# Performance work log

Hardware: AMD Instinct MI355X
Metric: run time of the kernel (lower is better)

Reference implementation:

```python
import jax, jax.numpy as jnp
import numpy as np


def _ragged_reverse(x, lengths):
    # x: [N, L, C]; flip the first `lengths[n]` steps of each sample, zero-fill the rest.
    N, L, C = x.shape
    t = jnp.arange(L, dtype=lengths.dtype)[None, :]          # [1, L]
    Ln = lengths[:, None]                                     # [N, 1]
    valid = t < Ln                                            # [N, L]
    idx = jnp.where(valid, Ln - 1 - t, 0)                     # [N, L]
    rev = jnp.take_along_axis(x, idx[:, :, None], axis=1)     # [N, L, C]
    return jnp.where(valid[:, :, None], rev, jnp.zeros((), x.dtype))


def _gru(xb, W_ih, W_hh, b_ih, b_hh):
    # xb: [B, L, C] -> outputs [B, L, H] (standard torch GRU cell math).
    B, L, C = xb.shape
    H = W_hh.shape[0]
    xw = xb @ W_ih + b_ih                                     # [B, L, 3H], input proj done once

    def step(h, xw_t):
        gh = h @ W_hh + b_hh                                  # [B, 3H]
        xr, xz, xn = jnp.split(xw_t, 3, axis=-1)
        hr, hz, hn = jnp.split(gh, 3, axis=-1)
        r = jax.nn.sigmoid(xr + hr)
        z = jax.nn.sigmoid(xz + hz)
        n = jnp.tanh(xn + r * hn)
        h_new = (1.0 - z) * n + z * h
        return h_new, h_new

    h0 = jnp.zeros((B, H), xb.dtype)
    _, ys = jax.lax.scan(step, h0, jnp.swapaxes(xw, 0, 1))    # ys: [L, B, H]
    return jnp.swapaxes(ys, 0, 1)                             # [B, L, H]


def reference(x, lengths, W_ih, W_hh, b_ih, b_hh):
    N, L, C = x.shape
    # to_bidirection: stack [forward; ragged-reversed] along batch -> [2N, L, C]
    rev = _ragged_reverse(x, lengths)
    xb = jnp.concatenate([x, rev], axis=0)
    out = _gru(xb, W_ih, W_hh, b_ih, b_hh)                    # [2N, L, H]
    # from_bidirection: split halves, concat on feature dim -> [N, L, 2H]
    return jnp.concatenate([out[:N], out[N:]], axis=2)


def setup_inputs() -> dict:
    key = jax.random.key(0)
    ks = jax.random.split(key, 6)
    N, L, C, H = 32, 2048, 64, 128
    s = 1.0 / np.sqrt(H)
    return {
        "x": jax.random.normal(ks[0], (N, L, C), dtype=jnp.float32),
        "lengths": jax.random.randint(ks[1], (N,), 1, L + 1, dtype=jnp.int32),
        "W_ih": jax.random.normal(ks[2], (C, 3 * H), dtype=jnp.float32) * s,
        "W_hh": jax.random.normal(ks[3], (H, 3 * H), dtype=jnp.float32) * s,
        "b_ih": jax.random.normal(ks[4], (3 * H,), dtype=jnp.float32) * s,
        "b_hh": jax.random.normal(ks[5], (3 * H,), dtype=jnp.float32) * s,
    }
```

## Files before the change

kernel.cpp:

```cpp
#include <hip/hip_runtime.h>

#define L_SEQ 2048
#define C_IN  64
#define HH    128
#define NSEQ  32
#define B2    64
#define G3    384
#define T_TILE 128

typedef _Float16 half2_t __attribute__((ext_vector_type(2)));

#define PINU(v) asm volatile("" : "+v"(v))

__device__ __forceinline__ float fdot2u(unsigned int a, unsigned int b, float c) {
    return __builtin_amdgcn_fdot2(__builtin_bit_cast(half2_t, a),
                                  __builtin_bit_cast(half2_t, b), c, false);
}

__device__ __forceinline__ unsigned int pack_h2(float a, float b) {
    half2_t t; t.x = (_Float16)a; t.y = (_Float16)b;
    return __builtin_bit_cast(unsigned int, t);
}

__device__ __forceinline__ float qadd1(float x) {
    int t = __builtin_amdgcn_update_dpp(0, __builtin_bit_cast(int, x),
                                        0xB1, 0xF, 0xF, true);
    return x + __builtin_bit_cast(float, t);
}

__device__ __forceinline__ float fast_sigmoid(float x) {
    float e = __builtin_amdgcn_exp2f(-1.4426950408889634f * x);
    return __builtin_amdgcn_rcpf(1.0f + e);
}

__device__ __forceinline__ float fast_tanh(float x) {
    float a = fabsf(x);
    float e = __builtin_amdgcn_exp2f(-2.8853900817779268f * a);
    float r = (1.0f - e) * __builtin_amdgcn_rcpf(1.0f + e);
    return copysignf(r, x);
}

__global__ __launch_bounds__(384) __attribute__((amdgpu_waves_per_eu(2, 2)))
void xw_kernel(const float* __restrict__ x, const int* __restrict__ lengths,
               const float* __restrict__ W_ih, const float* __restrict__ b_ih,
               const float* __restrict__ b_hh,
               float* __restrict__ xw, int t0, int chunk_steps)
{
    const int tid = threadIdx.x;
    const int tilesPerSeq = chunk_steps / T_TILE;
    const int s    = blockIdx.x / tilesPerSeq;
    const int tile = blockIdx.x % tilesPerSeq;
    const int tbase = t0 + tile * T_TILE;

    const bool isFwd = (s < NSEQ);
    const int  len   = isFwd ? L_SEQ : lengths[s - NSEQ];
    const float* __restrict__ xseq = x + (size_t)(s % NSEQ) * L_SEQ * C_IN;

    const int j = tid;
    float w[64];
#pragma unroll
    for (int q = 0; q < 64; ++q) w[q] = W_ih[q * G3 + j];
#pragma unroll
    for (int q = 0; q < 64; ++q) PINU(w[q]);
    const float bias = b_ih[j] + ((j < 256) ? b_hh[j] : 0.f);

    const int tloc = tile * T_TILE;
#pragma unroll 4
    for (int r = 0; r < T_TILE; ++r) {
        const int t = tbase + r;
        const int src = isFwd ? t : (len - 1 - t);
        float acc = bias;
        if (src >= 0) {
            const float* __restrict__ xrow = xseq + (size_t)src * C_IN;
#pragma unroll
            for (int q = 0; q < 64; ++q) acc += xrow[q] * w[q];
        }
        xw[((size_t)s * chunk_steps + (tloc + r)) * G3 + j] = acc;
    }
}

__global__ __launch_bounds__(256) __attribute__((amdgpu_waves_per_eu(1, 1)))
void gru_kernel(const float* __restrict__ xw, const float* __restrict__ W_hh,
                const float* __restrict__ b_hh, float* __restrict__ out,
                float* __restrict__ hstate, int t0, int chunk_steps)
{
    __shared__ unsigned int hbufu[2][64];
    const int s   = blockIdx.x;
    const int tid = threadIdx.x;
    const int j   = tid >> 1;
    const int p   = tid & 1;

    unsigned int wr[32], wz[32], wn[32];
    const float* Wb = W_hh + (size_t)(64 * p) * G3;
#pragma unroll
    for (int q = 0; q < 32; ++q) {
        wr[q] = pack_h2(Wb[(2*q) * G3 + j],       Wb[(2*q+1) * G3 + j]);
        wz[q] = pack_h2(Wb[(2*q) * G3 + 128 + j], Wb[(2*q+1) * G3 + 128 + j]);
        wn[q] = pack_h2(Wb[(2*q) * G3 + 256 + j], Wb[(2*q+1) * G3 + 256 + j]);
    }
#pragma unroll
    for (int q = 0; q < 32; ++q) { PINU(wr[q]); PINU(wz[q]); PINU(wn[q]); }
    float bn = b_hh[256 + j];
    PINU(bn);

    float hreg = (t0 == 0) ? 0.f : hstate[s * HH + j];
    if (tid < HH) {
        const float hv = (t0 == 0) ? 0.f : hstate[s * HH + tid];
        ((_Float16*)&hbufu[0][0])[tid] = (_Float16)hv;
    }
    __syncthreads();

    const float* xwp = xw + (size_t)s * chunk_steps * G3;
    float cr[4], cz[4], cn[4];
#pragma unroll
    for (int u = 0; u < 4; ++u) {
        const float* qp = xwp + (size_t)u * G3;
        cr[u] = qp[j]; cz[u] = qp[128 + j]; cn[u] = qp[256 + j];
    }

    float* outbase = out + (size_t)(s % NSEQ) * L_SEQ * 256 + ((s < NSEQ) ? 0 : HH);
    int cur = 0;

    for (int t = 0; t < chunk_steps; t += 4) {
        const int tnb = (t + 4 < chunk_steps) ? (t + 4) : t;
        float nr[4], nz[4], nn[4];
#pragma unroll
        for (int u = 0; u < 4; ++u) {
            const float* qp = xwp + (size_t)(tnb + u) * G3;
            nr[u] = qp[j]; nz[u] = qp[128 + j]; nn[u] = qp[256 + j];
        }

#pragma unroll
        for (int u = 0; u < 4; ++u) {
            float ar = 0.f, az = 0.f, an = 0.f;
            const uint4* hb = (const uint4*)&hbufu[cur][p * 32];
#pragma unroll
            for (int i = 0; i < 8; ++i) {
                const uint4 hv = hb[i];
                ar = fdot2u(hv.x, wr[4*i+0], ar); ar = fdot2u(hv.y, wr[4*i+1], ar);
                ar = fdot2u(hv.z, wr[4*i+2], ar); ar = fdot2u(hv.w, wr[4*i+3], ar);
                az = fdot2u(hv.x, wz[4*i+0], az); az = fdot2u(hv.y, wz[4*i+1], az);
                az = fdot2u(hv.z, wz[4*i+2], az); az = fdot2u(hv.w, wz[4*i+3], az);
                an = fdot2u(hv.x, wn[4*i+0], an); an = fdot2u(hv.y, wn[4*i+1], an);
                an = fdot2u(hv.z, wn[4*i+2], an); an = fdot2u(hv.w, wn[4*i+3], an);
            }
            ar = qadd1(ar);
            az = qadd1(az);
            an = qadd1(an);

            const float r = fast_sigmoid(cr[u] + ar);
            const float z = fast_sigmoid(cz[u] + az);
            const float n = fast_tanh(cn[u] + r * (an + bn));
            const float hnew = z * (hreg - n) + n;
            hreg = hnew;

            if (p == 0) {
                ((_Float16*)&hbufu[cur ^ 1][0])[j] = (_Float16)hnew;
                outbase[(size_t)(t0 + t + u) * 256 + j] = hnew;
            }
            asm volatile("s_waitcnt lgkmcnt(0)\n\ts_barrier" ::: "memory");
            cur ^= 1;
        }
#pragma unroll
        for (int u = 0; u < 4; ++u) { cr[u] = nr[u]; cz[u] = nz[u]; cn[u] = nn[u]; }
    }

    if (t0 + chunk_steps < L_SEQ && p == 0) hstate[s * HH + j] = hreg;
}

extern "C" void kernel_launch(void* const* d_in, const int* in_sizes, int n_in,
                              void* d_out, int out_size, void* d_ws, size_t ws_size,
                              hipStream_t stream) {
    const float* x       = (const float*)d_in[0];
    const int*   lengths = (const int*)  d_in[1];
    const float* W_ih    = (const float*)d_in[2];
    const float* W_hh    = (const float*)d_in[3];
    const float* b_ih    = (const float*)d_in[4];
    const float* b_hh    = (const float*)d_in[5];
    float* out = (float*)d_out;

    float* hstate = (float*)d_ws;
    float* xw     = hstate + B2 * HH;
    const size_t per_step = (size_t)B2 * G3 * sizeof(float);
    size_t avail = (ws_size > (size_t)B2 * HH * sizeof(float))
                 ? ws_size - (size_t)B2 * HH * sizeof(float) : 0;
    long long csteps = (long long)(avail / per_step);
    int chunk;
    if (csteps >= L_SEQ)       chunk = L_SEQ;
    else if (csteps >= T_TILE) chunk = (int)((csteps / T_TILE) * T_TILE);
    else                       chunk = T_TILE;

    for (int t0 = 0; t0 < L_SEQ; t0 += chunk) {
        const int steps = (L_SEQ - t0 < chunk) ? (L_SEQ - t0) : chunk;
        xw_kernel<<<dim3((steps / T_TILE) * B2), dim3(384), 0, stream>>>(
            x, lengths, W_ih, b_ih, b_hh, xw, t0, steps);
        gru_kernel<<<dim3(B2), dim3(256), 0, stream>>>(
            xw, W_hh, b_hh, out, hstate, t0, steps);
    }
}
```

Measured before the change: 1.104 ms.

## Pack two GRU sequences per workgroup and relax xw kernel occupancy hint

The recurrent GRU kernel now runs two independent sequences per 512-thread workgroup (32 blocks instead of 64), each with its own double-buffered hidden state in shared memory. The idea is to use fewer CUs with more waves each, so latency can be hidden across two sequences. The cost is that one barrier now synchronizes both sequences, and fewer CUs are active. The xw kernel's waves-per-EU hint is also removed.

```diff
diff --git a/kernel.cpp b/kernel.cpp
--- a/kernel.cpp
+++ b/kernel.cpp
@@ -40,7 +40,7 @@
     return copysignf(r, x);
 }
 
-__global__ __launch_bounds__(384) __attribute__((amdgpu_waves_per_eu(2, 2)))
+__global__ __launch_bounds__(384)
 void xw_kernel(const float* __restrict__ x, const int* __restrict__ lengths,
                const float* __restrict__ W_ih, const float* __restrict__ b_ih,
                const float* __restrict__ b_hh,
@@ -79,34 +79,36 @@
     }
 }
 
-__global__ __launch_bounds__(256) __attribute__((amdgpu_waves_per_eu(1, 1)))
+__global__ __launch_bounds__(512) __attribute__((amdgpu_waves_per_eu(2, 2)))
 void gru_kernel(const float* __restrict__ xw, const float* __restrict__ W_hh,
                 const float* __restrict__ b_hh, float* __restrict__ out,
                 float* __restrict__ hstate, int t0, int chunk_steps)
 {
-    __shared__ unsigned int hbufu[2][64];
-    const int s   = blockIdx.x;
+    __shared__ unsigned int hbufu[2][2][64];
     const int tid = threadIdx.x;
-    const int j   = tid >> 1;
-    const int p   = tid & 1;
+    const int q   = tid >> 8;
+    const int tl  = tid & 255;
+    const int s   = blockIdx.x * 2 + q;
+    const int j   = tl >> 1;
+    const int p   = tl & 1;
 
     unsigned int wr[32], wz[32], wn[32];
     const float* Wb = W_hh + (size_t)(64 * p) * G3;
 #pragma unroll
-    for (int q = 0; q < 32; ++q) {
-        wr[q] = pack_h2(Wb[(2*q) * G3 + j],       Wb[(2*q+1) * G3 + j]);
-        wz[q] = pack_h2(Wb[(2*q) * G3 + 128 + j], Wb[(2*q+1) * G3 + 128 + j]);
-        wn[q] = pack_h2(Wb[(2*q) * G3 + 256 + j], Wb[(2*q+1) * G3 + 256 + j]);
-    }
-#pragma unroll
-    for (int q = 0; q < 32; ++q) { PINU(wr[q]); PINU(wz[q]); PINU(wn[q]); }
+    for (int k = 0; k < 32; ++k) {
+        wr[k] = pack_h2(Wb[(2*k) * G3 + j],       Wb[(2*k+1) * G3 + j]);
+        wz[k] = pack_h2(Wb[(2*k) * G3 + 128 + j], Wb[(2*k+1) * G3 + 128 + j]);
+        wn[k] = pack_h2(Wb[(2*k) * G3 + 256 + j], Wb[(2*k+1) * G3 + 256 + j]);
+    }
+#pragma unroll
+    for (int k = 0; k < 32; ++k) { PINU(wr[k]); PINU(wz[k]); PINU(wn[k]); }
     float bn = b_hh[256 + j];
     PINU(bn);
 
     float hreg = (t0 == 0) ? 0.f : hstate[s * HH + j];
-    if (tid < HH) {
-        const float hv = (t0 == 0) ? 0.f : hstate[s * HH + tid];
-        ((_Float16*)&hbufu[0][0])[tid] = (_Float16)hv;
+    if (tl < HH) {
+        const float hv = (t0 == 0) ? 0.f : hstate[s * HH + tl];
+        ((_Float16*)&hbufu[q][0][0])[tl] = (_Float16)hv;
     }
     __syncthreads();
 
@@ -133,7 +135,7 @@
 #pragma unroll
         for (int u = 0; u < 4; ++u) {
             float ar = 0.f, az = 0.f, an = 0.f;
-            const uint4* hb = (const uint4*)&hbufu[cur][p * 32];
+            const uint4* hb = (const uint4*)&hbufu[q][cur][p * 32];
 #pragma unroll
             for (int i = 0; i < 8; ++i) {
                 const uint4 hv = hb[i];
@@ -155,7 +157,7 @@
             hreg = hnew;
 
             if (p == 0) {
-                ((_Float16*)&hbufu[cur ^ 1][0])[j] = (_Float16)hnew;
+                ((_Float16*)&hbufu[q][cur ^ 1][0])[j] = (_Float16)hnew;
                 outbase[(size_t)(t0 + t + u) * 256 + j] = hnew;
             }
             asm volatile("s_waitcnt lgkmcnt(0)\n\ts_barrier" ::: "memory");
@@ -194,7 +196,7 @@
         const int steps = (L_SEQ - t0 < chunk) ? (L_SEQ - t0) : chunk;
         xw_kernel<<<dim3((steps / T_TILE) * B2), dim3(384), 0, stream>>>(
             x, lengths, W_ih, b_ih, b_hh, xw, t0, steps);
-        gru_kernel<<<dim3(B2), dim3(256), 0, stream>>>(
+        gru_kernel<<<dim3(B2 / 2), dim3(512), 0, stream>>>(
             xw, W_hh, b_hh, out, hstate, t0, steps);
     }
 }
```

Result: slower. 1.476 ms (+33.6%).

## Fuse input projection into recurrent GRU kernel with producer warps and LDS ring

Applied to the files above, without the earlier changes.

Replaces the separate input-projection kernel and the global xw buffer with one kernel per sequence in which 256 producer threads compute x·W_ih (fp16 dot2) into a 16-slot LDS ring a few steps ahead. The other 256 consumer threads run the recurrence. This removes the global write and read of the projected activations and the second kernel launch. The cost is a larger block whose barriers now cover producer threads, and input projection at fp16 precision. The step loop is unrolled by two and the prefetch distance is fixed.

```diff
diff --git a/kernel.cpp b/kernel.cpp
--- a/kernel.cpp
+++ b/kernel.cpp
@@ -6,11 +6,12 @@
 #define NSEQ  32
 #define B2    64
 #define G3    384
-#define T_TILE 128
+#define RING  16
 
 typedef _Float16 half2_t __attribute__((ext_vector_type(2)));
 
 #define PINU(v) asm volatile("" : "+v"(v))
+#define STEP_BARRIER() asm volatile("s_waitcnt lgkmcnt(0)\n\ts_barrier" ::: "memory")
 
 __device__ __forceinline__ float fdot2u(unsigned int a, unsigned int b, float c) {
     return __builtin_amdgcn_fdot2(__builtin_bit_cast(half2_t, a),
@@ -40,132 +41,191 @@
     return copysignf(r, x);
 }
 
-__global__ __launch_bounds__(384) __attribute__((amdgpu_waves_per_eu(2, 2)))
-void xw_kernel(const float* __restrict__ x, const int* __restrict__ lengths,
-               const float* __restrict__ W_ih, const float* __restrict__ b_ih,
-               const float* __restrict__ b_hh,
-               float* __restrict__ xw, int t0, int chunk_steps)
+__device__ __forceinline__ float pdot32(const unsigned int (&w)[32],
+                                        const unsigned int* xrow, float acc) {
+    const uint4* x4 = (const uint4*)xrow;
+#pragma unroll
+    for (int i = 0; i < 8; ++i) {
+        const uint4 v = x4[i];
+        acc = fdot2u(v.x, w[4*i+0], acc);
+        acc = fdot2u(v.y, w[4*i+1], acc);
+        acc = fdot2u(v.z, w[4*i+2], acc);
+        acc = fdot2u(v.w, w[4*i+3], acc);
+    }
+    return acc;
+}
+
+__global__ __launch_bounds__(512) __attribute__((amdgpu_waves_per_eu(1, 1)))
+void bigru_fused(const float* __restrict__ x, const int* __restrict__ lengths,
+                 const float* __restrict__ W_ih, const float* __restrict__ W_hh,
+                 const float* __restrict__ b_ih, const float* __restrict__ b_hh,
+                 float* __restrict__ out)
 {
+    __shared__ unsigned int hbufu[2][64];
+    __shared__ float        ring[RING][G3];
+    __shared__ unsigned int xstage[2][2][32];
+
     const int tid = threadIdx.x;
-    const int tilesPerSeq = chunk_steps / T_TILE;
-    const int s    = blockIdx.x / tilesPerSeq;
-    const int tile = blockIdx.x % tilesPerSeq;
-    const int tbase = t0 + tile * T_TILE;
-
+    const int s   = blockIdx.x;
     const bool isFwd = (s < NSEQ);
     const int  len   = isFwd ? L_SEQ : lengths[s - NSEQ];
     const float* __restrict__ xseq = x + (size_t)(s % NSEQ) * L_SEQ * C_IN;
 
-    const int j = tid;
-    float w[64];
-#pragma unroll
-    for (int q = 0; q < 64; ++q) w[q] = W_ih[q * G3 + j];
-#pragma unroll
-    for (int q = 0; q < 64; ++q) PINU(w[q]);
-    const float bias = b_ih[j] + ((j < 256) ? b_hh[j] : 0.f);
-
-    const int tloc = tile * T_TILE;
-#pragma unroll 4
-    for (int r = 0; r < T_TILE; ++r) {
-        const int t = tbase + r;
-        const int src = isFwd ? t : (len - 1 - t);
-        float acc = bias;
-        if (src >= 0) {
-            const float* __restrict__ xrow = xseq + (size_t)src * C_IN;
-#pragma unroll
-            for (int q = 0; q < 64; ++q) acc += xrow[q] * w[q];
-        }
-        xw[((size_t)s * chunk_steps + (tloc + r)) * G3 + j] = acc;
-    }
-}
-
-__global__ __launch_bounds__(256) __attribute__((amdgpu_waves_per_eu(1, 1)))
-void gru_kernel(const float* __restrict__ xw, const float* __restrict__ W_hh,
-                const float* __restrict__ b_hh, float* __restrict__ out,
-                float* __restrict__ hstate, int t0, int chunk_steps)
-{
-    __shared__ unsigned int hbufu[2][64];
-    const int s   = blockIdx.x;
-    const int tid = threadIdx.x;
-    const int j   = tid >> 1;
-    const int p   = tid & 1;
-
-    unsigned int wr[32], wz[32], wn[32];
-    const float* Wb = W_hh + (size_t)(64 * p) * G3;
-#pragma unroll
-    for (int q = 0; q < 32; ++q) {
-        wr[q] = pack_h2(Wb[(2*q) * G3 + j],       Wb[(2*q+1) * G3 + j]);
-        wz[q] = pack_h2(Wb[(2*q) * G3 + 128 + j], Wb[(2*q+1) * G3 + 128 + j]);
-        wn[q] = pack_h2(Wb[(2*q) * G3 + 256 + j], Wb[(2*q+1) * G3 + 256 + j]);
-    }
-#pragma unroll
-    for (int q = 0; q < 32; ++q) { PINU(wr[q]); PINU(wz[q]); PINU(wn[q]); }
-    float bn = b_hh[256 + j];
-    PINU(bn);
-
-    float hreg = (t0 == 0) ? 0.f : hstate[s * HH + j];
-    if (tid < HH) {
-        const float hv = (t0 == 0) ? 0.f : hstate[s * HH + tid];
-        ((_Float16*)&hbufu[0][0])[tid] = (_Float16)hv;
-    }
-    __syncthreads();
-
-    const float* xwp = xw + (size_t)s * chunk_steps * G3;
-    float cr[4], cz[4], cn[4];
-#pragma unroll
-    for (int u = 0; u < 4; ++u) {
-        const float* qp = xwp + (size_t)u * G3;
-        cr[u] = qp[j]; cz[u] = qp[128 + j]; cn[u] = qp[256 + j];
-    }
-
-    float* outbase = out + (size_t)(s % NSEQ) * L_SEQ * 256 + ((s < NSEQ) ? 0 : HH);
+    const bool consumer = (tid < 256);
+    const int u = tid & 255;
+    const int j = u >> 1;
+    const int p = u & 1;
+
+    unsigned int w0[32], w1[32], w2[32];
+    float bA = 0.f, bB = 0.f;
+
+    if (consumer) {
+        const float* Wb = W_hh + (size_t)(64 * p) * G3;
+#pragma unroll
+        for (int k = 0; k < 32; ++k) {
+            w0[k] = pack_h2(Wb[(2*k) * G3 + j],       Wb[(2*k+1) * G3 + j]);
+            w1[k] = pack_h2(Wb[(2*k) * G3 + 128 + j], Wb[(2*k+1) * G3 + 128 + j]);
+            w2[k] = pack_h2(Wb[(2*k) * G3 + 256 + j], Wb[(2*k+1) * G3 + 256 + j]);
+        }
+#pragma unroll
+        for (int k = 0; k < 32; ++k) { PINU(w0[k]); PINU(w1[k]); PINU(w2[k]); }
+        bA = b_hh[256 + j];
+        if (tid < 64) hbufu[0][tid] = 0u;
+    } else {
+#pragma unroll
+        for (int k = 0; k < 32; ++k)
+            w0[k] = pack_h2(W_ih[(2*k) * G3 + u], W_ih[(2*k+1) * G3 + u]);
+        bA = b_ih[u] + b_hh[u];
+        if (u >= 128) {
+            const int c1 = 128 + u;
+#pragma unroll
+            for (int k = 0; k < 32; ++k)
+                w1[k] = pack_h2(W_ih[(2*k) * G3 + c1], W_ih[(2*k+1) * G3 + c1]);
+            bB = b_ih[c1];
+        }
+#pragma unroll
+        for (int k = 0; k < 32; ++k) { PINU(w0[k]); PINU(w1[k]); }
+    }
+
+    float2 xv = make_float2(0.f, 0.f);
+
+    for (int pg = 0; pg < 4; ++pg) {
+        if (!consumer && u < 64) {
+            const int rowIdx = 2 * pg + (u >= 32 ? 1 : 0);
+            const int e = u & 31;
+            const int srcL = isFwd ? rowIdx : (len - 1 - rowIdx);
+            float2 v = make_float2(0.f, 0.f);
+            if (srcL >= 0) v = *(const float2*)&xseq[(size_t)srcL * C_IN + 2*e];
+            xstage[pg & 1][(u >= 32) ? 1 : 0][e] = pack_h2(v.x, v.y);
+        }
+        __syncthreads();
+        if (!consumer && pg < 3) {
+            const unsigned int* xsA = &xstage[pg & 1][0][0];
+            const unsigned int* xsB = &xstage[pg & 1][1][0];
+            ring[2*pg][u]     = pdot32(w0, xsA, bA);
+            ring[2*pg + 1][u] = pdot32(w0, xsB, bA);
+            if (u >= 128) {
+                ring[2*pg][128 + u]     = pdot32(w1, xsA, bB);
+                ring[2*pg + 1][128 + u] = pdot32(w1, xsB, bB);
+            }
+        }
+        __syncthreads();
+    }
+
+    float cr = 0.f, cz = 0.f, cn = 0.f, nr = 0.f, nz = 0.f, nn = 0.f;
+    float hreg = 0.f;
+    if (consumer) { cr = ring[0][j]; cz = ring[0][128 + j]; cn = ring[0][256 + j]; }
+
+    float* outbase = out + (size_t)(s % NSEQ) * L_SEQ * 256 + (isFwd ? 0 : HH);
     int cur = 0;
 
-    for (int t = 0; t < chunk_steps; t += 4) {
-        const int tnb = (t + 4 < chunk_steps) ? (t + 4) : t;
-        float nr[4], nz[4], nn[4];
-#pragma unroll
-        for (int u = 0; u < 4; ++u) {
-            const float* qp = xwp + (size_t)(tnb + u) * G3;
-            nr[u] = qp[j]; nz[u] = qp[128 + j]; nn[u] = qp[256 + j];
-        }
-
-#pragma unroll
-        for (int u = 0; u < 4; ++u) {
+    for (int g = 0; g < L_SEQ / 2; ++g) {
+        const int tA = 2 * g;
+        if (consumer) {
+            const int sln = (tA + 1) & (RING - 1);
+            nr = ring[sln][j]; nz = ring[sln][128 + j]; nn = ring[sln][256 + j];
             float ar = 0.f, az = 0.f, an = 0.f;
             const uint4* hb = (const uint4*)&hbufu[cur][p * 32];
 #pragma unroll
             for (int i = 0; i < 8; ++i) {
                 const uint4 hv = hb[i];
-                ar = fdot2u(hv.x, wr[4*i+0], ar); ar = fdot2u(hv.y, wr[4*i+1], ar);
-                ar = fdot2u(hv.z, wr[4*i+2], ar); ar = fdot2u(hv.w, wr[4*i+3], ar);
-                az = fdot2u(hv.x, wz[4*i+0], az); az = fdot2u(hv.y, wz[4*i+1], az);
-                az = fdot2u(hv.z, wz[4*i+2], az); az = fdot2u(hv.w, wz[4*i+3], az);
-                an = fdot2u(hv.x, wn[4*i+0], an); an = fdot2u(hv.y, wn[4*i+1], an);
-                an = fdot2u(hv.z, wn[4*i+2], an); an = fdot2u(hv.w, wn[4*i+3], an);
-            }
-            ar = qadd1(ar);
-            az = qadd1(az);
-            an = qadd1(an);
-
-            const float r = fast_sigmoid(cr[u] + ar);
-            const float z = fast_sigmoid(cz[u] + az);
-            const float n = fast_tanh(cn[u] + r * (an + bn));
+                ar = fdot2u(hv.x, w0[4*i+0], ar); ar = fdot2u(hv.y, w0[4*i+1], ar);
+                ar = fdot2u(hv.z, w0[4*i+2], ar); ar = fdot2u(hv.w, w0[4*i+3], ar);
+                az = fdot2u(hv.x, w1[4*i+0], az); az = fdot2u(hv.y, w1[4*i+1], az);
+                az = fdot2u(hv.z, w1[4*i+2], az); az = fdot2u(hv.w, w1[4*i+3], az);
+                an = fdot2u(hv.x, w2[4*i+0], an); an = fdot2u(hv.y, w2[4*i+1], an);
+                an = fdot2u(hv.z, w2[4*i+2], an); an = fdot2u(hv.w, w2[4*i+3], an);
+            }
+            ar = qadd1(ar); az = qadd1(az); an = qadd1(an);
+            const float r = fast_sigmoid(cr + ar);
+            const float z = fast_sigmoid(cz + az);
+            const float n = fast_tanh(cn + r * (an + bA));
             const float hnew = z * (hreg - n) + n;
             hreg = hnew;
-
             if (p == 0) {
                 ((_Float16*)&hbufu[cur ^ 1][0])[j] = (_Float16)hnew;
-                outbase[(size_t)(t0 + t + u) * 256 + j] = hnew;
-            }
-            asm volatile("s_waitcnt lgkmcnt(0)\n\ts_barrier" ::: "memory");
+                outbase[(size_t)tA * 256 + j] = hnew;
+            }
             cur ^= 1;
-        }
-#pragma unroll
-        for (int u = 0; u < 4; ++u) { cr[u] = nr[u]; cz[u] = nz[u]; cn[u] = nn[u]; }
-    }
-
-    if (t0 + chunk_steps < L_SEQ && p == 0) hstate[s * HH + j] = hreg;
+        } else {
+            const int rdA = tA + 6;
+            if (rdA < L_SEQ) {
+                const unsigned int* xsA = &xstage[(g + 1) & 1][0][0];
+                const unsigned int* xsB = &xstage[(g + 1) & 1][1][0];
+                const int slA = rdA & (RING - 1), slB = (rdA + 1) & (RING - 1);
+                ring[slA][u] = pdot32(w0, xsA, bA);
+                ring[slB][u] = pdot32(w0, xsB, bA);
+                if (u >= 128) {
+                    ring[slA][128 + u] = pdot32(w1, xsA, bB);
+                    ring[slB][128 + u] = pdot32(w1, xsB, bB);
+                }
+            }
+            const int rl = tA + 8;
+            if (u < 64 && rl < L_SEQ) {
+                const int rowIdx = rl + (u >= 32 ? 1 : 0);
+                const int e = u & 31;
+                const int srcL = isFwd ? rowIdx : (len - 1 - rowIdx);
+                xv = make_float2(0.f, 0.f);
+                if (srcL >= 0) xv = *(const float2*)&xseq[(size_t)srcL * C_IN + 2*e];
+            }
+        }
+        STEP_BARRIER();
+        {
+            const int tB = tA + 1;
+            if (consumer) {
+                const int sln = (tB + 1) & (RING - 1);
+                cr = ring[sln][j]; cz = ring[sln][128 + j]; cn = ring[sln][256 + j];
+                float ar = 0.f, az = 0.f, an = 0.f;
+                const uint4* hb = (const uint4*)&hbufu[cur][p * 32];
+#pragma unroll
+                for (int i = 0; i < 8; ++i) {
+                    const uint4 hv = hb[i];
+                    ar = fdot2u(hv.x, w0[4*i+0], ar); ar = fdot2u(hv.y, w0[4*i+1], ar);
+                    ar = fdot2u(hv.z, w0[4*i+2], ar); ar = fdot2u(hv.w, w0[4*i+3], ar);
+                    az = fdot2u(hv.x, w1[4*i+0], az); az = fdot2u(hv.y, w1[4*i+1], az);
+                    az = fdot2u(hv.z, w1[4*i+2], az); az = fdot2u(hv.w, w1[4*i+3], az);
+                    an = fdot2u(hv.x, w2[4*i+0], an); an = fdot2u(hv.y, w2[4*i+1], an);
+                    an = fdot2u(hv.z, w2[4*i+2], an); an = fdot2u(hv.w, w2[4*i+3], an);
+                }
+                ar = qadd1(ar); az = qadd1(az); an = qadd1(an);
+                const float r = fast_sigmoid(nr + ar);
+                const float z = fast_sigmoid(nz + az);
+                const float n = fast_tanh(nn + r * (an + bA));
+                const float hnew = z * (hreg - n) + n;
+                hreg = hnew;
+                if (p == 0) {
+                    ((_Float16*)&hbufu[cur ^ 1][0])[j] = (_Float16)hnew;
+                    outbase[(size_t)tB * 256 + j] = hnew;
+                }
+                cur ^= 1;
+            } else {
+                if (u < 64 && tA + 8 < L_SEQ) {
+                    xstage[g & 1][(u >= 32) ? 1 : 0][u & 31] = pack_h2(xv.x, xv.y);
+                }
+            }
+        }
+        STEP_BARRIER();
+    }
 }
 
 extern "C" void kernel_launch(void* const* d_in, const int* in_sizes, int n_in,
@@ -179,22 +239,6 @@
     const float* b_hh    = (const float*)d_in[5];
     float* out = (float*)d_out;
 
-    float* hstate = (float*)d_ws;
-    float* xw     = hstate + B2 * HH;
-    const size_t per_step = (size_t)B2 * G3 * sizeof(float);
-    size_t avail = (ws_size > (size_t)B2 * HH * sizeof(float))
-                 ? ws_size - (size_t)B2 * HH * sizeof(float) : 0;
-    long long csteps = (long long)(avail / per_step);
-    int chunk;
-    if (csteps >= L_SEQ)       chunk = L_SEQ;
-    else if (csteps >= T_TILE) chunk = (int)((csteps / T_TILE) * T_TILE);
-    else                       chunk = T_TILE;
-
-    for (int t0 = 0; t0 < L_SEQ; t0 += chunk) {
-        const int steps = (L_SEQ - t0 < chunk) ? (L_SEQ - t0) : chunk;
-        xw_kernel<<<dim3((steps / T_TILE) * B2), dim3(384), 0, stream>>>(
-            x, lengths, W_ih, b_ih, b_hh, xw, t0, steps);
-        gru_kernel<<<dim3(B2), dim3(256), 0, stream>>>(
-            xw, W_hh, b_hh, out, hstate, t0, steps);
-    }
-}
+    bigru_fused<<<dim3(B2), dim3(512), 0, stream>>>(
+        x, lengths, W_ih, W_hh, b_ih, b_hh, out);
+}
```

Measured after the change: 1.151 ms. +4.3%, slower.

## Compute GRU hidden matvec with MFMA instead of packed fp16 dot products

Applied to the files above, without the earlier changes.

Replaces the per-thread fdot2 recurrent matvec with 16x16x32 f16 MFMA instructions, holding W_hh fragments in registers and reading the broadcast hidden row from LDS as the A operand. Each wave computes 32 output columns for all three gates, and the cross-lane DPP reduction is dropped. The xw prefetch changes from a 4-step batch to a one-step lookahead, and the waves-per-EU hint on the input projection kernel is removed. Most MFMA output rows are discarded and the dependent MFMA chains add latency to the sequential step.

```diff
diff --git a/kernel.cpp b/kernel.cpp
--- a/kernel.cpp
+++ b/kernel.cpp
@@ -8,31 +8,17 @@
 #define G3    384
 #define T_TILE 128
 
-typedef _Float16 half2_t __attribute__((ext_vector_type(2)));
+typedef _Float16 f16x8 __attribute__((ext_vector_type(8)));
+typedef float    f32x4 __attribute__((ext_vector_type(4)));
 
 #define PINU(v) asm volatile("" : "+v"(v))
-
-__device__ __forceinline__ float fdot2u(unsigned int a, unsigned int b, float c) {
-    return __builtin_amdgcn_fdot2(__builtin_bit_cast(half2_t, a),
-                                  __builtin_bit_cast(half2_t, b), c, false);
-}
-
-__device__ __forceinline__ unsigned int pack_h2(float a, float b) {
-    half2_t t; t.x = (_Float16)a; t.y = (_Float16)b;
-    return __builtin_bit_cast(unsigned int, t);
-}
-
-__device__ __forceinline__ float qadd1(float x) {
-    int t = __builtin_amdgcn_update_dpp(0, __builtin_bit_cast(int, x),
-                                        0xB1, 0xF, 0xF, true);
-    return x + __builtin_bit_cast(float, t);
-}
+#define STEP_BARRIER() asm volatile("s_waitcnt lgkmcnt(0)\n\ts_barrier" ::: "memory")
+#define MFMA16(a, b, c) __builtin_amdgcn_mfma_f32_16x16x32_f16((a), (b), (c), 0, 0, 0)
 
 __device__ __forceinline__ float fast_sigmoid(float x) {
     float e = __builtin_amdgcn_exp2f(-1.4426950408889634f * x);
     return __builtin_amdgcn_rcpf(1.0f + e);
 }
-
 __device__ __forceinline__ float fast_tanh(float x) {
     float a = fabsf(x);
     float e = __builtin_amdgcn_exp2f(-2.8853900817779268f * a);
@@ -40,7 +26,7 @@
     return copysignf(r, x);
 }
 
-__global__ __launch_bounds__(384) __attribute__((amdgpu_waves_per_eu(2, 2)))
+__global__ __launch_bounds__(384)
 void xw_kernel(const float* __restrict__ x, const int* __restrict__ lengths,
                const float* __restrict__ W_ih, const float* __restrict__ b_ih,
                const float* __restrict__ b_hh,
@@ -80,92 +66,115 @@
 }
 
 __global__ __launch_bounds__(256) __attribute__((amdgpu_waves_per_eu(1, 1)))
-void gru_kernel(const float* __restrict__ xw, const float* __restrict__ W_hh,
-                const float* __restrict__ b_hh, float* __restrict__ out,
-                float* __restrict__ hstate, int t0, int chunk_steps)
+void gru_mfma(const float* __restrict__ xw, const float* __restrict__ W_hh,
+              const float* __restrict__ b_hh, float* __restrict__ out,
+              float* __restrict__ hstate, int t0, int chunk_steps)
 {
-    __shared__ unsigned int hbufu[2][64];
+    __shared__ _Float16 hrow[2][HH];
+
     const int s   = blockIdx.x;
     const int tid = threadIdx.x;
-    const int j   = tid >> 1;
-    const int p   = tid & 1;
-
-    unsigned int wr[32], wz[32], wn[32];
-    const float* Wb = W_hh + (size_t)(64 * p) * G3;
-#pragma unroll
-    for (int q = 0; q < 32; ++q) {
-        wr[q] = pack_h2(Wb[(2*q) * G3 + j],       Wb[(2*q+1) * G3 + j]);
-        wz[q] = pack_h2(Wb[(2*q) * G3 + 128 + j], Wb[(2*q+1) * G3 + 128 + j]);
-        wn[q] = pack_h2(Wb[(2*q) * G3 + 256 + j], Wb[(2*q+1) * G3 + 256 + j]);
-    }
-#pragma unroll
-    for (int q = 0; q < 32; ++q) { PINU(wr[q]); PINU(wz[q]); PINU(wn[q]); }
-    float bn = b_hh[256 + j];
-    PINU(bn);
-
-    float hreg = (t0 == 0) ? 0.f : hstate[s * HH + j];
-    if (tid < HH) {
-        const float hv = (t0 == 0) ? 0.f : hstate[s * HH + tid];
-        ((_Float16*)&hbufu[0][0])[tid] = (_Float16)hv;
+    const int w   = tid >> 6;
+    const int l   = tid & 63;
+    const int lm  = l & 15;
+    const int lg  = l >> 4;
+    const int col0 = 32 * w + lm;
+    const int col1 = col0 + 16;
+    const bool fwd = (s < NSEQ);
+
+    f16x8 Br[2][4], Bz[2][4], Bn[2][4];
+#pragma unroll
+    for (int e = 0; e < 2; ++e) {
+        const int col = 32 * w + 16 * e + lm;
+#pragma unroll
+        for (int kt = 0; kt < 4; ++kt) {
+            f16x8 fr, fz, fn;
+#pragma unroll
+            for (int i = 0; i < 8; ++i) {
+                const int k = kt * 32 + lg * 8 + i;
+                fr[i] = (_Float16)W_hh[k * G3 + col];
+                fz[i] = (_Float16)W_hh[k * G3 + 128 + col];
+                fn[i] = (_Float16)W_hh[k * G3 + 256 + col];
+            }
+            Br[e][kt] = fr; Bz[e][kt] = fz; Bn[e][kt] = fn;
+        }
+    }
+    const float bn0 = b_hh[256 + col0];
+    const float bn1 = b_hh[256 + col1];
+
+    float ho0, ho1;
+    if (t0 == 0) {
+        ho0 = 0.f; ho1 = 0.f;
+        if (tid < HH) hrow[0][tid] = (_Float16)0.f;
+    } else {
+        ho0 = hstate[s * HH + col0];
+        ho1 = hstate[s * HH + col1];
+        if (tid < HH) hrow[0][tid] = (_Float16)hstate[s * HH + tid];
     }
     __syncthreads();
 
     const float* xwp = xw + (size_t)s * chunk_steps * G3;
-    float cr[4], cz[4], cn[4];
-#pragma unroll
-    for (int u = 0; u < 4; ++u) {
-        const float* qp = xwp + (size_t)u * G3;
-        cr[u] = qp[j]; cz[u] = qp[128 + j]; cn[u] = qp[256 + j];
-    }
-
-    float* outbase = out + (size_t)(s % NSEQ) * L_SEQ * 256 + ((s < NSEQ) ? 0 : HH);
+    float cr0 = xwp[col0], cz0 = xwp[128 + col0], cn0 = xwp[256 + col0];
+    float cr1 = xwp[col1], cz1 = xwp[128 + col1], cn1 = xwp[256 + col1];
+
+    float* outbase = out + (size_t)(s % NSEQ) * L_SEQ * 256 + (fwd ? 0 : HH);
     int cur = 0;
 
-    for (int t = 0; t < chunk_steps; t += 4) {
-        const int tnb = (t + 4 < chunk_steps) ? (t + 4) : t;
-        float nr[4], nz[4], nn[4];
-#pragma unroll
-        for (int u = 0; u < 4; ++u) {
-            const float* qp = xwp + (size_t)(tnb + u) * G3;
-            nr[u] = qp[j]; nz[u] = qp[128 + j]; nn[u] = qp[256 + j];
+    for (int t = 0; t < chunk_steps; ++t) {
+        const uint4* hb = (const uint4*)&hrow[cur][0];
+        const f16x8 A0 = __builtin_bit_cast(f16x8, hb[0 * 4 + lg]);
+        const f16x8 A1 = __builtin_bit_cast(f16x8, hb[1 * 4 + lg]);
+        const f16x8 A2 = __builtin_bit_cast(f16x8, hb[2 * 4 + lg]);
+        const f16x8 A3 = __builtin_bit_cast(f16x8, hb[3 * 4 + lg]);
+
+        const int tn = (t + 1 < chunk_steps) ? (t + 1) : t;
+        const float* qp = xwp + (size_t)tn * G3;
+        const float nr0 = qp[col0], nz0 = qp[128 + col0], nn0 = qp[256 + col0];
+        const float nr1 = qp[col1], nz1 = qp[128 + col1], nn1 = qp[256 + col1];
+
+        f32x4 ar0 = {0.f,0.f,0.f,0.f}, az0 = {0.f,0.f,0.f,0.f}, an0 = {0.f,0.f,0.f,0.f};
+        f32x4 ar1 = {0.f,0.f,0.f,0.f}, az1 = {0.f,0.f,0.f,0.f}, an1 = {0.f,0.f,0.f,0.f};
+        ar0 = MFMA16(A0, Br[0][0], ar0); ar0 = MFMA16(A1, Br[0][1], ar0);
+        ar0 = MFMA16(A2, Br[0][2], ar0); ar0 = MFMA16(A3, Br[0][3], ar0);
+        az0 = MFMA16(A0, Bz[0][0], az0); az0 = MFMA16(A1, Bz[0][1], az0);
+        az0 = MFMA16(A2, Bz[0][2], az0); az0 = MFMA16(A3, Bz[0][3], az0);
+        an0 = MFMA16(A0, Bn[0][0], an0); an0 = MFMA16(A1, Bn[0][1], an0);
+        an0 = MFMA16(A2, Bn[0][2], an0); an0 = MFMA16(A3, Bn[0][3], an0);
+        ar1 = MFMA16(A0, Br[1][0], ar1); ar1 = MFMA16(A1, Br[1][1], ar1);
+        ar1 = MFMA16(A2, Br[1][2], ar1); ar1 = MFMA16(A3, Br[1][3], ar1);
+        az1 = MFMA16(A0, Bz[1][0], az1); az1 = MFMA16(A1, Bz[1][1], az1);
+        az1 = MFMA16(A2, Bz[1][2], az1); az1 = MFMA16(A3, Bz[1][3], az1);
+        an1 = MFMA16(A0, Bn[1][0], an1); an1 = MFMA16(A1, Bn[1][1], an1);
+        an1 = MFMA16(A2, Bn[1][2], an1); an1 = MFMA16(A3, Bn[1][3], an1);
+
+        const float r0 = fast_sigmoid(cr0 + ar0[0]);
+        const float z0 = fast_sigmoid(cz0 + az0[0]);
+        const float n0 = fast_tanh(cn0 + r0 * (an0[0] + bn0));
+        const float h0 = z0 * (ho0 - n0) + n0;
+        ho0 = h0;
+        const float r1 = fast_sigmoid(cr1 + ar1[0]);
+        const float z1 = fast_sigmoid(cz1 + az1[0]);
+        const float n1 = fast_tanh(cn1 + r1 * (an1[0] + bn1));
+        const float h1 = z1 * (ho1 - n1) + n1;
+        ho1 = h1;
+
+        if (lg == 0) {
+            hrow[cur ^ 1][col0] = (_Float16)h0;
+            hrow[cur ^ 1][col1] = (_Float16)h1;
+            float* op = outbase + (size_t)(t0 + t) * 256;
+            op[col0] = h0;
+            op[col1] = h1;
         }
-
-#pragma unroll
-        for (int u = 0; u < 4; ++u) {
-            float ar = 0.f, az = 0.f, an = 0.f;
-            const uint4* hb = (const uint4*)&hbufu[cur][p * 32];
-#pragma unroll
-            for (int i = 0; i < 8; ++i) {
-                const uint4 hv = hb[i];
-                ar = fdot2u(hv.x, wr[4*i+0], ar); ar = fdot2u(hv.y, wr[4*i+1], ar);
-                ar = fdot2u(hv.z, wr[4*i+2], ar); ar = fdot2u(hv.w, wr[4*i+3], ar);
-                az = fdot2u(hv.x, wz[4*i+0], az); az = fdot2u(hv.y, wz[4*i+1], az);
-                az = fdot2u(hv.z, wz[4*i+2], az); az = fdot2u(hv.w, wz[4*i+3], az);
-                an = fdot2u(hv.x, wn[4*i+0], an); an = fdot2u(hv.y, wn[4*i+1], an);
-                an = fdot2u(hv.z, wn[4*i+2], an); an = fdot2u(hv.w, wn[4*i+3], an);
-            }
-            ar = qadd1(ar);
-            az = qadd1(az);
-            an = qadd1(an);
-
-            const float r = fast_sigmoid(cr[u] + ar);
-            const float z = fast_sigmoid(cz[u] + az);
-            const float n = fast_tanh(cn[u] + r * (an + bn));
-            const float hnew = z * (hreg - n) + n;
-            hreg = hnew;
-
-            if (p == 0) {
-                ((_Float16*)&hbufu[cur ^ 1][0])[j] = (_Float16)hnew;
-                outbase[(size_t)(t0 + t + u) * 256 + j] = hnew;
-            }
-            asm volatile("s_waitcnt lgkmcnt(0)\n\ts_barrier" ::: "memory");
-            cur ^= 1;
-        }
-#pragma unroll
-        for (int u = 0; u < 4; ++u) { cr[u] = nr[u]; cz[u] = nz[u]; cn[u] = nn[u]; }
-    }
-
-    if (t0 + chunk_steps < L_SEQ && p == 0) hstate[s * HH + j] = hreg;
+        STEP_BARRIER();
+        cur ^= 1;
+        cr0 = nr0; cz0 = nz0; cn0 = nn0;
+        cr1 = nr1; cz1 = nz1; cn1 = nn1;
+    }
+
+    if (t0 + chunk_steps < L_SEQ && lg == 0) {
+        hstate[s * HH + col0] = ho0;
+        hstate[s * HH + col1] = ho1;
+    }
 }
 
 extern "C" void kernel_launch(void* const* d_in, const int* in_sizes, int n_in,
@@ -194,7 +203,7 @@
         const int steps = (L_SEQ - t0 < chunk) ? (L_SEQ - t0) : chunk;
         xw_kernel<<<dim3((steps / T_TILE) * B2), dim3(384), 0, stream>>>(
             x, lengths, W_ih, b_ih, b_hh, xw, t0, steps);
-        gru_kernel<<<dim3(B2), dim3(256), 0, stream>>>(
+        gru_mfma<<<dim3(B2), dim3(256), 0, stream>>>(
             xw, W_hh, b_hh, out, hstate, t0, steps);
     }
 }
```

Result: slower. 1.173 ms (+6.3%).
